# Optimization experiments

Hardware: AMD Instinct MI355X
Metric: run time of the kernel (lower is better)

## Reference

```python
import jax, jax.numpy as jnp
import numpy as np

D_MODEL = 1024
NUM_HEADS = 16
HEAD_DIM = D_MODEL // NUM_HEADS


def setup_inputs() -> dict:
    key = jax.random.key(0)
    ks = jax.random.split(key, 9)
    B, S = 2, 2048
    s = 1.0 / np.sqrt(D_MODEL)
    return {
        "x": jax.random.normal(ks[0], (B, S, D_MODEL), dtype=jnp.float32),
        "Wq": jax.random.normal(ks[1], (D_MODEL, D_MODEL), dtype=jnp.float32) * s,
        "bq": jnp.zeros((D_MODEL,), dtype=jnp.float32),
        "Wk": jax.random.normal(ks[2], (D_MODEL, D_MODEL), dtype=jnp.float32) * s,
        "bk": jnp.zeros((D_MODEL,), dtype=jnp.float32),
        "Wv": jax.random.normal(ks[3], (D_MODEL, D_MODEL), dtype=jnp.float32) * s,
        "bv": jnp.zeros((D_MODEL,), dtype=jnp.float32),
        "Wo": jax.random.normal(ks[4], (D_MODEL, D_MODEL), dtype=jnp.float32) * s,
        "bo": jnp.zeros((D_MODEL,), dtype=jnp.float32),
    }


def reference(x, Wq, bq, Wk, bk, Wv, bv, Wo, bo):
    B, S, _ = x.shape
    # projections; weights stored as (in, out) so y = x @ W + b
    def heads(y):  # [B,S,D] -> [B,H,S,Dh]
        return y.reshape(B, S, NUM_HEADS, HEAD_DIM).transpose(0, 2, 1, 3)

    Q = heads(x @ Wq + bq)
    K = heads(x @ Wk + bk)
    V = heads(x @ Wv + bv)
    scale = 1.0 / np.sqrt(HEAD_DIM).astype(np.float32)
    scores = jnp.einsum("bhqd,bhkd->bhqk", Q, K) * scale  # [B,H,S,S]
    attn = jax.nn.softmax(scores, axis=-1)
    ctx = jnp.einsum("bhqk,bhkd->bhqd", attn, V)  # [B,H,S,Dh]
    ctx = ctx.transpose(0, 2, 1, 3).reshape(B, S, D_MODEL)
    return ctx @ Wo + bo
```

## Files before the change

kernel.cpp:

```cpp
#include <hip/hip_runtime.h>
#include <hip/hip_bf16.h>

#define SEQ   2048
#define NH    16
#define HD    64
#define DM    1024
#define MROWS 4096

#define QSCALE 0.1803368801111204f

typedef __attribute__((ext_vector_type(4))) float f32x4;
typedef __attribute__((ext_vector_type(8))) short s16x8;
typedef __attribute__((ext_vector_type(4))) short s16x4;

__device__ __forceinline__ short f2bf(float f) {
  union { float f; unsigned u; } v; v.f = f;
  return (short)((v.u + 0x7fff + ((v.u >> 16) & 1)) >> 16);
}

__device__ __forceinline__ unsigned pack2bf(float lo, float hi) {
  unsigned ul = __float_as_uint(lo) + 0x8000u;
  unsigned uh = __float_as_uint(hi) + 0x8000u;
  return __builtin_amdgcn_perm(uh, ul, 0x07060302u);
}

__device__ __forceinline__ void gload_lds16(const short* g, short* l) {
  __builtin_amdgcn_global_load_lds(
      (const __attribute__((address_space(1))) void*)g,
      (__attribute__((address_space(3))) void*)l, 16, 0, 0);
}

#define SWZ(row, gg) ((((row) << 3) + (((gg) ^ ((row) & 7)))) << 3)
#define SWZ16(row, gg) ((((row) << 4) + (((gg) ^ ((row) & 15)))) << 3)

__global__ void prep(const float* __restrict__ x, short* __restrict__ xb,
                     const float* __restrict__ Wq, const float* __restrict__ Wk,
                     const float* __restrict__ Wv, const float* __restrict__ Wo,
                     short* __restrict__ WT) {
  const int t = threadIdx.x;
  if (blockIdx.z == 4) {
    int c = blockIdx.y * 16 + blockIdx.x;
    #pragma unroll
    for (int itr = 0; itr < 8; ++itr) {
      int i = c * 16384 + itr * 2048 + t * 8;
      const float4* p = reinterpret_cast<const float4*>(x + i);
      float4 a = p[0], b = p[1];
      s16x8 o;
      o[0] = f2bf(a.x); o[1] = f2bf(a.y); o[2] = f2bf(a.z); o[3] = f2bf(a.w);
      o[4] = f2bf(b.x); o[5] = f2bf(b.y); o[6] = f2bf(b.z); o[7] = f2bf(b.w);
      *reinterpret_cast<s16x8*>(xb + i) = o;
    }
    return;
  }
  __shared__ float tile[64][65];
  const float* W = (blockIdx.z == 0) ? Wq : (blockIdx.z == 1) ? Wk : (blockIdx.z == 2) ? Wv : Wo;
  short* dst = WT + (size_t)blockIdx.z * DM * DM;
  int kbase = blockIdx.x * 64;
  int nbase = blockIdx.y * 64;
  {
    int n4 = (t & 15) * 4;
    #pragma unroll
    for (int rr = 0; rr < 4; ++rr) {
      int r = (t >> 4) + 16 * rr;
      float4 v = *reinterpret_cast<const float4*>(W + (size_t)(kbase + r) * DM + nbase + n4);
      tile[r][n4] = v.x; tile[r][n4 + 1] = v.y; tile[r][n4 + 2] = v.z; tile[r][n4 + 3] = v.w;
    }
  }
  __syncthreads();
  {
    int n = t >> 2, kc = (t & 3) * 16;
    short tmp[16];
    #pragma unroll
    for (int j = 0; j < 16; ++j) tmp[j] = f2bf(tile[kc + j][n]);
    s16x8* q = reinterpret_cast<s16x8*>(dst + (size_t)(nbase + n) * DM + kbase + kc);
    q[0] = *reinterpret_cast<s16x8*>(tmp);
    q[1] = *reinterpret_cast<s16x8*>(tmp + 8);
  }
}

__global__ __launch_bounds__(256, 2) void gemm_qkv(
    const short* __restrict__ A, const short* __restrict__ BT,
    const float* __restrict__ bias0, const float* __restrict__ bias1,
    const float* __restrict__ bias2,
    short* __restrict__ oQ, short* __restrict__ oK, short* __restrict__ oVt) {
  __shared__ __align__(16) short As[128 * 64];
  __shared__ __align__(16) short Bs[128 * 64];
  const int lin = blockIdx.x;
  const int wg = (lin & 7) * 96 + (lin >> 3);
  const int bx = wg & 31;
  const int by = wg >> 5;
  const int lane = threadIdx.x & 63;
  const int wid = threadIdx.x >> 6;
  const int q15 = lane & 15, g4 = lane >> 4;
  const int mbase = bx * 128;
  const int nbase = by * 128;
  const int wm = wid >> 1, wn = wid & 1;

  f32x4 acc[4][4] = {};
  const int srow = lane >> 3;
  const int sg = (lane & 7) ^ srow;

  for (int k0 = 0; k0 < DM; k0 += 64) {
    #pragma unroll
    for (int j = 0; j < 4; ++j) {
      int c = wid * 4 + j;
      int row = c * 8 + srow;
      gload_lds16(A + (size_t)(mbase + row) * DM + k0 + sg * 8, As + c * 512);
      gload_lds16(BT + (size_t)(nbase + row) * DM + k0 + sg * 8, Bs + c * 512);
    }
    __syncthreads();
    #pragma unroll
    for (int ks = 0; ks < 2; ++ks) {
      s16x8 af[4], bfr[4];
      #pragma unroll
      for (int m = 0; m < 4; ++m)
        af[m] = *reinterpret_cast<const s16x8*>(As + SWZ(wm * 64 + m * 16 + q15, ks * 4 + g4));
      #pragma unroll
      for (int n = 0; n < 4; ++n)
        bfr[n] = *reinterpret_cast<const s16x8*>(Bs + SWZ(wn * 64 + n * 16 + q15, ks * 4 + g4));
      #pragma unroll
      for (int m = 0; m < 4; ++m)
        #pragma unroll
        for (int n = 0; n < 4; ++n)
          acc[m][n] = __builtin_amdgcn_mfma_f32_16x16x32_bf16(af[m], bfr[n], acc[m][n], 0, 0, 0);
    }
    __syncthreads();
  }

  const int r0 = mbase + wm * 64;
  const int c0 = nbase + wn * 64;
  #pragma unroll
  for (int m = 0; m < 4; ++m) {
    #pragma unroll
    for (int n = 0; n < 4; ++n) {
      int rr = r0 + m * 16 + g4 * 4;
      int cc = c0 + n * 16 + q15;
      int seg = cc >> 10, c1 = cc & 1023;
      const float* bp = (seg == 0) ? bias0 : (seg == 1) ? bias1 : bias2;
      float bv = bp[c1];
      int h = c1 >> 6, d = c1 & 63;
      if (seg == 2) {
        s16x4 o;
        #pragma unroll
        for (int i = 0; i < 4; ++i) o[i] = f2bf(acc[m][n][i] + bv);
        int b = rr >> 11, s = rr & 2047;
        *reinterpret_cast<s16x4*>(
            oVt + ((size_t)(b * NH + h) * HD + d) * SEQ + s) = o;
      } else {
        short* dst = (seg == 0) ? oQ : oK;
        #pragma unroll
        for (int i = 0; i < 4; ++i) {
          int r = rr + i;
          float v = acc[m][n][i] + bv;
          if (seg == 0) v *= QSCALE;
          int b = r >> 11, s = r & 2047;
          size_t idx = (((size_t)(b * NH + h) * SEQ + s) << 6) + d;
          dst[idx] = f2bf(v);
        }
      }
    }
  }
}

__global__ __launch_bounds__(256, 2) void gemm_o(
    const short* __restrict__ A, const short* __restrict__ BT,
    const float* __restrict__ bias, float* __restrict__ oF) {
  __shared__ __align__(16) short As[64 * 128];
  __shared__ __align__(16) short Bs[128 * 128];
  const int lin = blockIdx.x;
  const int wg = (lin & 7) * 64 + (lin >> 3);
  const int bx = wg & 63;
  const int by = wg >> 6;
  const int lane = threadIdx.x & 63;
  const int wid = threadIdx.x >> 6;
  const int q15 = lane & 15, g4 = lane >> 4;
  const int mbase = bx * 64;
  const int nbase = by * 128;
  const int t = threadIdx.x;
  const int wbase = t & 448;

  f32x4 acc[4][2] = {};

  for (int k0 = 0; k0 < DM; k0 += 128) {
    #pragma unroll
    for (int l = 0; l < 4; ++l) {
      int glin = l * 256 + t;
      int row = glin >> 4, gg = glin & 15;
      int sgg = gg ^ (row & 15);
      gload_lds16(A + (size_t)(mbase + row) * DM + k0 + sgg * 8,
                  As + (l * 256 + wbase) * 8);
    }
    #pragma unroll
    for (int l = 0; l < 8; ++l) {
      int glin = l * 256 + t;
      int row = glin >> 4, gg = glin & 15;
      int sgg = gg ^ (row & 15);
      gload_lds16(BT + (size_t)(nbase + row) * DM + k0 + sgg * 8,
                  Bs + (l * 256 + wbase) * 8);
    }
    __syncthreads();
    #pragma unroll
    for (int ks = 0; ks < 4; ++ks) {
      s16x8 af[4], bfr[2];
      #pragma unroll
      for (int m = 0; m < 4; ++m)
        af[m] = *reinterpret_cast<const s16x8*>(As + SWZ16(m * 16 + q15, ks * 4 + g4));
      #pragma unroll
      for (int n = 0; n < 2; ++n)
        bfr[n] = *reinterpret_cast<const s16x8*>(Bs + SWZ16(wid * 32 + n * 16 + q15, ks * 4 + g4));
      #pragma unroll
      for (int m = 0; m < 4; ++m)
        #pragma unroll
        for (int n = 0; n < 2; ++n)
          acc[m][n] = __builtin_amdgcn_mfma_f32_16x16x32_bf16(af[m], bfr[n], acc[m][n], 0, 0, 0);
    }
    __syncthreads();
  }

  #pragma unroll
  for (int m = 0; m < 4; ++m) {
    #pragma unroll
    for (int n = 0; n < 2; ++n) {
      int cc = nbase + wid * 32 + n * 16 + q15;
      float bv = bias[cc];
      #pragma unroll
      for (int i = 0; i < 4; ++i) {
        int r = mbase + m * 16 + g4 * 4 + i;
        oF[(size_t)r * DM + cc] = acc[m][n][i] + bv;
      }
    }
  }
}

__global__ __launch_bounds__(512, 4) void attn(const short* __restrict__ Q,
                                               const short* __restrict__ K,
                                               const short* __restrict__ Vt,
                                               short* __restrict__ ctx) {
  const int bh = blockIdx.y;
  const int lane = threadIdx.x & 63;
  const int wid = threadIdx.x >> 6;
  const int q15 = lane & 15, g4 = lane >> 4;
  const int qrow = blockIdx.x * 128 + wid * 16;
  const short* Qh = Q + (size_t)bh * SEQ * HD;
  const short* Kh = K + (size_t)bh * SEQ * HD;
  const short* Vh = Vt + (size_t)bh * HD * SEQ;

  __shared__ __align__(16) short Ks[2][64 * 64];
  __shared__ __align__(16) short Vs[2][64 * 64];
  __shared__ __align__(16) short Plds[8][16][72];
  short(*P)[72] = Plds[wid];

  const int t = threadIdx.x;
  const int srow = t >> 3;
  const int sg = (t & 7) ^ (srow & 7);
  const short* ksrc = Kh + (size_t)srow * HD + sg * 8;
  const short* vsrc = Vh + (size_t)srow * SEQ + sg * 8;

  s16x8 qf[2];
  #pragma unroll
  for (int ks = 0; ks < 2; ++ks)
    qf[ks] = *reinterpret_cast<const s16x8*>(
        Qh + (size_t)(qrow + q15) * HD + ks * 32 + g4 * 8);

  s16x8 ones;
  #pragma unroll
  for (int i = 0; i < 8; ++i) ones[i] = (short)0x3F80;

  f32x4 acco[4] = {};
  f32x4 lacc = {};
  float mrun = 0.f;

  gload_lds16(ksrc, Ks[0] + wid * 512);
  gload_lds16(vsrc, Vs[0] + wid * 512);
  __syncthreads();

  int cur = 0;
  for (int it = 0; it < SEQ / 64; ++it) {
    if (it + 1 < SEQ / 64) {
      gload_lds16(ksrc + (size_t)(it + 1) * 64 * HD, Ks[cur ^ 1] + wid * 512);
      gload_lds16(vsrc + (it + 1) * 64, Vs[cur ^ 1] + wid * 512);
    }
    const short* Kb = Ks[cur];
    const short* Vb = Vs[cur];

    f32x4 sacc[4] = {};
    #pragma unroll
    for (int kb = 0; kb < 4; ++kb) {
      s16x8 kf0 = *reinterpret_cast<const s16x8*>(Kb + SWZ(kb * 16 + q15, g4));
      s16x8 kf1 = *reinterpret_cast<const s16x8*>(Kb + SWZ(kb * 16 + q15, g4 + 4));
      sacc[kb] = __builtin_amdgcn_mfma_f32_16x16x32_bf16(kf0, qf[0], sacc[kb], 0, 0, 0);
      sacc[kb] = __builtin_amdgcn_mfma_f32_16x16x32_bf16(kf1, qf[1], sacc[kb], 0, 0, 0);
    }

    if (it == 0) {
      float t0 = fmaxf(fmaxf(sacc[0][0], sacc[0][1]), fmaxf(sacc[0][2], sacc[0][3]));
      float t1 = fmaxf(fmaxf(sacc[1][0], sacc[1][1]), fmaxf(sacc[1][2], sacc[1][3]));
      float t2 = fmaxf(fmaxf(sacc[2][0], sacc[2][1]), fmaxf(sacc[2][2], sacc[2][3]));
      float t3 = fmaxf(fmaxf(sacc[3][0], sacc[3][1]), fmaxf(sacc[3][2], sacc[3][3]));
      float tmax = fmaxf(fmaxf(t0, t1), fmaxf(t2, t3));
      float tm = fmaxf(tmax, __shfl_xor(tmax, 16));
      mrun = fmaxf(tm, __shfl_xor(tm, 32));
    }

    #pragma unroll
    for (int kb = 0; kb < 4; ++kb) {
      float p0 = __builtin_amdgcn_exp2f(sacc[kb][0] - mrun);
      float p1 = __builtin_amdgcn_exp2f(sacc[kb][1] - mrun);
      float p2 = __builtin_amdgcn_exp2f(sacc[kb][2] - mrun);
      float p3 = __builtin_amdgcn_exp2f(sacc[kb][3] - mrun);
      uint2 w;
      w.x = pack2bf(p0, p1);
      w.y = pack2bf(p2, p3);
      *reinterpret_cast<uint2*>(&P[q15][kb * 16 + g4 * 4]) = w;
    }
    s16x8 pf0 = *reinterpret_cast<const s16x8*>(&P[q15][g4 * 8]);
    s16x8 pf1 = *reinterpret_cast<const s16x8*>(&P[q15][32 + g4 * 8]);

    lacc = __builtin_amdgcn_mfma_f32_16x16x32_bf16(ones, pf0, lacc, 0, 0, 0);
    lacc = __builtin_amdgcn_mfma_f32_16x16x32_bf16(ones, pf1, lacc, 0, 0, 0);

    #pragma unroll
    for (int dvb = 0; dvb < 4; ++dvb) {
      s16x8 vf0 = *reinterpret_cast<const s16x8*>(Vb + SWZ(dvb * 16 + q15, g4));
      s16x8 vf1 = *reinterpret_cast<const s16x8*>(Vb + SWZ(dvb * 16 + q15, g4 + 4));
      acco[dvb] = __builtin_amdgcn_mfma_f32_16x16x32_bf16(vf0, pf0, acco[dvb], 0, 0, 0);
      acco[dvb] = __builtin_amdgcn_mfma_f32_16x16x32_bf16(vf1, pf1, acco[dvb], 0, 0, 0);
    }

    __syncthreads();
    cur ^= 1;
  }

  const int b = bh >> 4, h = bh & 15;
  float inv = 1.f / lacc[0];
  int q = qrow + q15;
  #pragma unroll
  for (int dvb = 0; dvb < 4; ++dvb) {
    s16x4 o;
    #pragma unroll
    for (int i = 0; i < 4; ++i) o[i] = f2bf(acco[dvb][i] * inv);
    int d = dvb * 16 + g4 * 4;
    *reinterpret_cast<s16x4*>(ctx + ((size_t)b * SEQ + q) * DM + h * HD + d) = o;
  }
}

extern "C" void kernel_launch(void* const* d_in, const int* in_sizes, int n_in,
                              void* d_out, int out_size, void* d_ws, size_t ws_size,
                              hipStream_t stream) {
  const float* x = (const float*)d_in[0];
  const float* Wq = (const float*)d_in[1];
  const float* bq = (const float*)d_in[2];
  const float* Wk = (const float*)d_in[3];
  const float* bk = (const float*)d_in[4];
  const float* Wv = (const float*)d_in[5];
  const float* bv = (const float*)d_in[6];
  const float* Wo = (const float*)d_in[7];
  const float* bo = (const float*)d_in[8];

  char* ws = (char*)d_ws;
  const size_t MB8 = (size_t)8 << 20;
  short* xb  = (short*)(ws);
  short* WT  = (short*)(ws + 1 * MB8);
  short* Qb  = (short*)(ws + 2 * MB8);
  short* Kb  = (short*)(ws + 3 * MB8);
  short* Vtb = (short*)(ws + 5 * MB8);
  short* ctx = (short*)(ws + 6 * MB8);

  prep<<<dim3(16, 16, 5), 256, 0, stream>>>(x, xb, Wq, Wk, Wv, Wo, WT);
  gemm_qkv<<<dim3(768), 256, 0, stream>>>(xb, WT, bq, bk, bv, Qb, Kb, Vtb);
  attn<<<dim3(SEQ / 128, 32), 512, 0, stream>>>(Qb, Kb, Vtb, ctx);
  gemm_o<<<dim3(512), 256, 0, stream>>>(ctx, WT + (size_t)3072 * DM, bo, (float*)d_out);
}
```

Baseline: 117.8 us.

## Software-pipeline attention loop: overlap PV of previous tile with QK of current

```diff
diff --git a/kernel.cpp b/kernel.cpp
--- a/kernel.cpp
+++ b/kernel.cpp
@@ -246,9 +246,8 @@
   const short* Vh = Vt + (size_t)bh * HD * SEQ;
 
   __shared__ __align__(16) short Ks[2][64 * 64];
-  __shared__ __align__(16) short Vs[2][64 * 64];
-  __shared__ __align__(16) short Plds[8][16][72];
-  short(*P)[72] = Plds[wid];
+  __shared__ __align__(16) short Vs[3][64 * 64];
+  __shared__ __align__(16) short Plds[8][2][16][72];
 
   const int t = threadIdx.x;
   const int srow = t >> 3;
@@ -274,15 +273,13 @@
   gload_lds16(vsrc, Vs[0] + wid * 512);
   __syncthreads();
 
-  int cur = 0;
   for (int it = 0; it < SEQ / 64; ++it) {
     if (it + 1 < SEQ / 64) {
-      gload_lds16(ksrc + (size_t)(it + 1) * 64 * HD, Ks[cur ^ 1] + wid * 512);
-      gload_lds16(vsrc + (it + 1) * 64, Vs[cur ^ 1] + wid * 512);
-    }
-    const short* Kb = Ks[cur];
-    const short* Vb = Vs[cur];
-
+      gload_lds16(ksrc + (size_t)(it + 1) * 64 * HD, Ks[(it + 1) & 1] + wid * 512);
+      gload_lds16(vsrc + (it + 1) * 64, Vs[(it + 1) % 3] + wid * 512);
+    }
+
+    const short* Kb = Ks[it & 1];
     f32x4 sacc[4] = {};
     #pragma unroll
     for (int kb = 0; kb < 4; ++kb) {
@@ -290,6 +287,22 @@
       s16x8 kf1 = *reinterpret_cast<const s16x8*>(Kb + SWZ(kb * 16 + q15, g4 + 4));
       sacc[kb] = __builtin_amdgcn_mfma_f32_16x16x32_bf16(kf0, qf[0], sacc[kb], 0, 0, 0);
       sacc[kb] = __builtin_amdgcn_mfma_f32_16x16x32_bf16(kf1, qf[1], sacc[kb], 0, 0, 0);
+    }
+
+    if (it > 0) {
+      short(*Pp)[72] = Plds[wid][(it - 1) & 1];
+      s16x8 pf0 = *reinterpret_cast<const s16x8*>(&Pp[q15][g4 * 8]);
+      s16x8 pf1 = *reinterpret_cast<const s16x8*>(&Pp[q15][32 + g4 * 8]);
+      lacc = __builtin_amdgcn_mfma_f32_16x16x32_bf16(ones, pf0, lacc, 0, 0, 0);
+      lacc = __builtin_amdgcn_mfma_f32_16x16x32_bf16(ones, pf1, lacc, 0, 0, 0);
+      const short* Vb = Vs[(it - 1) % 3];
+      #pragma unroll
+      for (int dvb = 0; dvb < 4; ++dvb) {
+        s16x8 vf0 = *reinterpret_cast<const s16x8*>(Vb + SWZ(dvb * 16 + q15, g4));
+        s16x8 vf1 = *reinterpret_cast<const s16x8*>(Vb + SWZ(dvb * 16 + q15, g4 + 4));
+        acco[dvb] = __builtin_amdgcn_mfma_f32_16x16x32_bf16(vf0, pf0, acco[dvb], 0, 0, 0);
+        acco[dvb] = __builtin_amdgcn_mfma_f32_16x16x32_bf16(vf1, pf1, acco[dvb], 0, 0, 0);
+      }
     }
 
     if (it == 0) {
@@ -302,6 +315,7 @@
       mrun = fmaxf(tm, __shfl_xor(tm, 32));
     }
 
+    short(*Pc)[72] = Plds[wid][it & 1];
     #pragma unroll
     for (int kb = 0; kb < 4; ++kb) {
       float p0 = __builtin_amdgcn_exp2f(sacc[kb][0] - mrun);
@@ -311,14 +325,20 @@
       uint2 w;
       w.x = pack2bf(p0, p1);
       w.y = pack2bf(p2, p3);
-      *reinterpret_cast<uint2*>(&P[q15][kb * 16 + g4 * 4]) = w;
-    }
-    s16x8 pf0 = *reinterpret_cast<const s16x8*>(&P[q15][g4 * 8]);
-    s16x8 pf1 = *reinterpret_cast<const s16x8*>(&P[q15][32 + g4 * 8]);
-
+      *reinterpret_cast<uint2*>(&Pc[q15][kb * 16 + g4 * 4]) = w;
+    }
+
+    __syncthreads();
+  }
+
+  {
+    constexpr int last = SEQ / 64 - 1;
+    short(*Pp)[72] = Plds[wid][last & 1];
+    s16x8 pf0 = *reinterpret_cast<const s16x8*>(&Pp[q15][g4 * 8]);
+    s16x8 pf1 = *reinterpret_cast<const s16x8*>(&Pp[q15][32 + g4 * 8]);
     lacc = __builtin_amdgcn_mfma_f32_16x16x32_bf16(ones, pf0, lacc, 0, 0, 0);
     lacc = __builtin_amdgcn_mfma_f32_16x16x32_bf16(ones, pf1, lacc, 0, 0, 0);
-
+    const short* Vb = Vs[last % 3];
     #pragma unroll
     for (int dvb = 0; dvb < 4; ++dvb) {
       s16x8 vf0 = *reinterpret_cast<const s16x8*>(Vb + SWZ(dvb * 16 + q15, g4));
@@ -326,9 +346,6 @@
       acco[dvb] = __builtin_amdgcn_mfma_f32_16x16x32_bf16(vf0, pf0, acco[dvb], 0, 0, 0);
       acco[dvb] = __builtin_amdgcn_mfma_f32_16x16x32_bf16(vf1, pf1, acco[dvb], 0, 0, 0);
     }
-
-    __syncthreads();
-    cur ^= 1;
   }
 
   const int b = bh >> 4, h = bh & 15;
```

After: 117.3 us. About the same (-0.4%).
